# Optimization experiments

Measured on AMD Instinct MI355X. Metric: run time of the kernel, lower is better.

The kernel has to match this reference:

```python
import jax, jax.numpy as jnp
import numpy as np

N_HEADS = 16
LEVELS = 3
DS = 2          # downsampling_factor
WINDOW = 128    # sliding window size
B, L, E = 32, 512, 1024


def _mha(q, k, v, Wq, bq, Wk, bk, Wv, bv, Wo, bo):
    """batch_first nn.MultiheadAttention equivalent (no mask)."""
    b, lq, e = q.shape
    lk = k.shape[1]
    d = e // N_HEADS
    scale = 1.0 / np.sqrt(d)
    qh = (q @ Wq + bq).reshape(b, lq, N_HEADS, d)
    kh = (k @ Wk + bk).reshape(b, lk, N_HEADS, d)
    vh = (v @ Wv + bv).reshape(b, lk, N_HEADS, d)
    att = jax.nn.softmax(jnp.einsum('bqhd,bkhd->bhqk', qh, kh) * scale, axis=-1)
    out = jnp.einsum('bhqk,bkhd->bqhd', att, vh).reshape(b, lq, e)
    return out @ Wo + bo


def _downsample(x):
    b, l, e = x.shape
    ln = l // DS
    return x[:, :ln * DS].reshape(b, ln, DS, e).mean(axis=2)


def setup_inputs() -> dict:
    key = jax.random.key(0)
    ks = jax.random.split(key, 8)
    s = E ** -0.5
    return {
        'query': jax.random.normal(ks[0], (B, L, E), jnp.float32),
        'key': jax.random.normal(ks[1], (B, L, E), jnp.float32),
        'value': jax.random.normal(ks[2], (B, L, E), jnp.float32),
        'Wq': jax.random.normal(ks[3], (E, E), jnp.float32) * s,
        'bq': jnp.zeros((E,), jnp.float32),
        'Wk': jax.random.normal(ks[4], (E, E), jnp.float32) * s,
        'bk': jnp.zeros((E,), jnp.float32),
        'Wv': jax.random.normal(ks[5], (E, E), jnp.float32) * s,
        'bv': jnp.zeros((E,), jnp.float32),
        'Wo': jax.random.normal(ks[6], (E, E), jnp.float32) * s,
        'bo': jnp.zeros((E,), jnp.float32),
        'soft_mask': jnp.ones((L,), jnp.float32),
    }


def reference(query, key, value, Wq, bq, Wk, bk, Wv, bv, Wo, bo, soft_mask):
    params = (Wq, bq, Wk, bk, Wv, bv, Wo, bo)
    # hierarchical multi-scale attention: full KV + (levels-1) downsampled KVs
    k, v = key, value
    acc = _mha(query, k, v, *params)
    for _ in range(LEVELS - 1):
        k = _downsample(k)
        v = _downsample(v)
        acc = acc + _mha(query, k, v, *params)
    hier = acc / LEVELS
    # sliding-window local attention (L divisible by WINDOW)
    b, l, e = query.shape
    nw = l // WINDOW
    qw = query.reshape(b * nw, WINDOW, e)
    kw = key.reshape(b * nw, WINDOW, e)
    vw = value.reshape(b * nw, WINDOW, e)
    sw = _mha(qw, kw, vw, *params).reshape(b, l, e)
    # soft mask gating
    sm = jax.nn.sigmoid(soft_mask[:l])
    return (hier + sw) * sm[None, :, None]
```

## Files before the change

### kernel.cpp

```cpp
#include <hip/hip_runtime.h>

#define EDIM 1024
#define MROWS 16384
#define DHEAD 64
#define LSEQ 512
#define NT 16

typedef unsigned short u16;
typedef unsigned int u32;
typedef __bf16 bf16x8 __attribute__((ext_vector_type(8)));
typedef unsigned short u16x8 __attribute__((ext_vector_type(8)));
typedef float f32x4 __attribute__((ext_vector_type(4)));

__device__ __forceinline__ u16 f2bf(float x) {
    return __builtin_bit_cast(u16, (__bf16)x);
}
__device__ __forceinline__ float bf2f(u16 h) {
    return __builtin_bit_cast(float, (u32)h << 16);
}
__device__ __forceinline__ bf16x8 ld8(const u16* p) {
    return __builtin_bit_cast(bf16x8, *(const u16x8*)p);
}
__device__ __forceinline__ bf16x8 ld8s(const u16* base, int row, int koff) {
    return ld8((const u16*)((const char*)base + row * 128 + ((koff * 2) ^ ((row & 7) << 4))));
}
__device__ __forceinline__ bf16x8 ld8v(const u16* base, int c, int koff) {
    return ld8((const u16*)((const char*)base + c * 128 + ((koff * 2) ^ (((c >> 2) & 7) << 4))));
}
__device__ __forceinline__ void glds16(const u16* g, u16* l) {
    __builtin_amdgcn_global_load_lds(
        (const __attribute__((address_space(1))) u32*)g,
        (__attribute__((address_space(3))) u32*)l, 16, 0, 0);
}
#define MFMA(a, b, c) __builtin_amdgcn_mfma_f32_16x16x32_bf16((a), (b), (c), 0, 0, 0)
#define U4C(v, i) ((i) == 0 ? (v).x : (i) == 1 ? (v).y : (i) == 2 ? (v).z : (v).w)
#define VMCNT(n) asm volatile("s_waitcnt vmcnt(" #n ")" ::: "memory")
#define SBAR()   __builtin_amdgcn_s_barrier()

__global__ __launch_bounds__(256) void prep_wt_kernel(
    const float* __restrict__ Wq, const float* __restrict__ Wk,
    const float* __restrict__ Wv, const float* __restrict__ Wo,
    u16* __restrict__ WTh)
{
    const int z = blockIdx.z;
    const float* W = (z == 0) ? Wq : (z == 1) ? Wk : (z == 2) ? Wv : Wo;
    u16* th = WTh + (size_t)z * EDIM * EDIM;
    const int k0 = blockIdx.x * 64, n0 = blockIdx.y * 64;
    __shared__ float tile[64][65];
    for (int i = threadIdx.x; i < 4096; i += 256) {
        int r = i >> 6, c = i & 63;
        tile[r][c] = W[(size_t)(k0 + r) * EDIM + n0 + c];
    }
    __syncthreads();
    for (int i = threadIdx.x; i < 4096; i += 256) {
        int r = i >> 6, c = i & 63;
        th[(size_t)(n0 + r) * EDIM + k0 + c] = f2bf(tile[c][r]);
    }
}

__global__ __launch_bounds__(256) void convert_kernel(
    const float* __restrict__ Aq, const float* __restrict__ Ak, const float* __restrict__ Av,
    u16* __restrict__ Dq, u16* __restrict__ Dk, u16* __restrict__ Dv)
{
    const int z = blockIdx.z;
    const float* src = (z == 0) ? Aq : (z == 1) ? Ak : Av;
    u16* dst = (z == 0) ? Dq : (z == 1) ? Dk : Dv;
    const size_t total8 = (size_t)MROWS * EDIM / 8;
    for (size_t i = (size_t)blockIdx.x * 256 + threadIdx.x; i < total8;
         i += (size_t)gridDim.x * 256) {
        const float4 a = *(const float4*)&src[i * 8];
        const float4 b = *(const float4*)&src[i * 8 + 4];
        ushort4 h0, h1;
        h0.x = f2bf(a.x); h0.y = f2bf(a.y); h0.z = f2bf(a.z); h0.w = f2bf(a.w);
        h1.x = f2bf(b.x); h1.y = f2bf(b.y); h1.z = f2bf(b.z); h1.w = f2bf(b.w);
        *(ushort4*)&dst[i * 8]     = h0;
        *(ushort4*)&dst[i * 8 + 4] = h1;
    }
}

template<int EPI>
__global__ __launch_bounds__(512, 1) void gemm256(
    const u16* __restrict__ A, const u16* __restrict__ BT,
    const float* __restrict__ bias,
    u16* __restrict__ Ch, float* __restrict__ Cf, const float* __restrict__ smask)
{
    extern __shared__ u16 lds[];
    const int tid = threadIdx.x;
    const int lane = tid & 63, w = tid >> 6;
    const int wm = w >> 2, wn = w & 3;
    const int lr = lane & 15, lg = lane >> 4;
    int D = blockIdx.x;
    int T = (D & 7) * 32 + (D >> 3);
    const int m0 = (T >> 2) * 256, n0 = (T & 3) * 256;

    u16* As0 = lds;
    u16* As1 = lds + 16384;
    u16* Bs0 = lds + 32768;
    u16* Bs1 = lds + 49152;

    auto stageB = [&](int bf, int t) {
        u16* dst = bf ? Bs1 : Bs0;
        #pragma unroll
        for (int c = 0; c < 4; ++c) {
            int idx = tid + c * 512;
            int row = idx >> 3, ch = idx & 7, sch = ch ^ (row & 7);
            glds16(&BT[(size_t)(n0 + row) * EDIM + t * 64 + sch * 8], dst + idx * 8);
        }
    };
    auto stageA = [&](int bf, int t) {
        u16* dst = bf ? As1 : As0;
        #pragma unroll
        for (int c = 0; c < 4; ++c) {
            int idx = tid + c * 512;
            int row = idx >> 3, ch = idx & 7, sch = ch ^ (row & 7);
            glds16(&A[(size_t)(m0 + row) * EDIM + t * 64 + sch * 8], dst + idx * 8);
        }
    };

    f32x4 acc[8][4] = {};
    bf16x8 bf0[4], bf1[4];

    stageB(0, 0);
    stageA(0, 0);
    VMCNT(0);
    SBAR();
    #pragma unroll
    for (int n = 0; n < 4; ++n)
        bf0[n] = ld8s(Bs0, wn * 64 + n * 16 + lr, lg * 8);

    for (int t = 0; t < NT; ++t) {
        const int cur = t & 1;
        u16* Asc = cur ? As1 : As0;
        u16* Bsc = cur ? Bs1 : Bs0;
        u16* Bsn = cur ? Bs0 : Bs1;
        const bool more = (t + 1 < NT);
        bf16x8 af[4];
        #pragma unroll
        for (int mm = 0; mm < 4; ++mm)
            af[mm] = ld8s(Asc, wm * 128 + mm * 16 + lr, lg * 8);
        if (more) { stageB(cur ^ 1, t + 1); stageA(cur ^ 1, t + 1); }
        SBAR();
        __builtin_amdgcn_s_setprio(1);
        #pragma unroll
        for (int n = 0; n < 4; ++n)
            #pragma unroll
            for (int mm = 0; mm < 4; ++mm)
                acc[mm][n] = MFMA(af[mm], bf0[n], acc[mm][n]);
        __builtin_amdgcn_s_setprio(0);
        SBAR();
        bf16x8 ag[4];
        #pragma unroll
        for (int mm = 0; mm < 4; ++mm)
            ag[mm] = ld8s(Asc, wm * 128 + 64 + mm * 16 + lr, lg * 8);
        SBAR();
        __builtin_amdgcn_s_setprio(1);
        #pragma unroll
        for (int n = 0; n < 4; ++n)
            #pragma unroll
            for (int mm = 0; mm < 4; ++mm)
                acc[4 + mm][n] = MFMA(ag[mm], bf0[n], acc[4 + mm][n]);
        __builtin_amdgcn_s_setprio(0);
        SBAR();
        #pragma unroll
        for (int mm = 0; mm < 4; ++mm)
            af[mm] = ld8s(Asc, wm * 128 + mm * 16 + lr, 32 + lg * 8);
        #pragma unroll
        for (int n = 0; n < 4; ++n)
            bf1[n] = ld8s(Bsc, wn * 64 + n * 16 + lr, 32 + lg * 8);
        SBAR();
        __builtin_amdgcn_s_setprio(1);
        #pragma unroll
        for (int n = 0; n < 4; ++n)
            #pragma unroll
            for (int mm = 0; mm < 4; ++mm)
                acc[mm][n] = MFMA(af[mm], bf1[n], acc[mm][n]);
        __builtin_amdgcn_s_setprio(0);
        VMCNT(4);
        SBAR();
        #pragma unroll
        for (int mm = 0; mm < 4; ++mm)
            ag[mm] = ld8s(Asc, wm * 128 + 64 + mm * 16 + lr, 32 + lg * 8);
        if (more) {
            #pragma unroll
            for (int n = 0; n < 4; ++n)
                bf0[n] = ld8s(Bsn, wn * 64 + n * 16 + lr, lg * 8);
        }
        SBAR();
        __builtin_amdgcn_s_setprio(1);
        #pragma unroll
        for (int n = 0; n < 4; ++n)
            #pragma unroll
            for (int mm = 0; mm < 4; ++mm)
                acc[4 + mm][n] = MFMA(ag[mm], bf1[n], acc[4 + mm][n]);
        __builtin_amdgcn_s_setprio(0);
        VMCNT(0);
        SBAR();
    }
    #pragma unroll
    for (int m = 0; m < 8; ++m)
        #pragma unroll
        for (int n = 0; n < 4; ++n) {
            int col = n0 + wn * 64 + n * 16 + lr;
            float bc = bias[col];
            #pragma unroll
            for (int r = 0; r < 4; ++r) {
                int row = m0 + wm * 128 + m * 16 + lg * 4 + r;
                float x = acc[m][n][r];
                if (EPI == 1) {
                    float g = 1.0f / (1.0f + __expf(-smask[row & (LSEQ - 1)]));
                    Cf[(size_t)row * EDIM + col] = (x + 2.0f * bc) * g;
                } else {
                    Ch[(size_t)row * EDIM + col] = f2bf(x + bc);
                }
            }
        }
}

__global__ __launch_bounds__(256, 2) void attn_kernel(
    const u16* __restrict__ Q, const u16* __restrict__ K,
    const u16* __restrict__ V, u16* __restrict__ ctx)
{
    const int tid = threadIdx.x, lane = tid & 63, w = tid >> 6;
    const int lr = lane & 15, lg = lane >> 4;
    int D = (blockIdx.z * gridDim.y + blockIdx.y) * gridDim.x + blockIdx.x;
    int T = (D & 7) * 512 + (D >> 3);
    const int qq = T & 7, hd = (T >> 3) & 15, b = T >> 7;
    const int wrow = b * LSEQ + qq * 64 + w * 16;
    const int ecol = hd * DHEAD;
    const int kvbase = b * LSEQ;
    const int wt0 = qq & ~1;

    __shared__ u16 Ks[2][64 * 64];
    __shared__ u16 Vt[64 * 64];
    __shared__ u16 Ps[4][3 * 16 * 72];

    u16* psw = &Ps[w][0];

    bf16x8 qf0 = ld8(&Q[(size_t)(wrow + lr) * EDIM + ecol + lg * 8]);
    bf16x8 qf1 = ld8(&Q[(size_t)(wrow + lr) * EDIM + ecol + 32 + lg * 8]);

    f32x4 o0[4] = {}, o1[4] = {}, o2[4] = {}, ow[4] = {};
    float l0 = 0, l1 = 0, l2 = 0, lw = 0;
    ushort4 vr[2][2];

    auto issueK = [&](int t, int bf) {
        #pragma unroll
        for (int c = 0; c < 2; ++c) {
            int idx = tid + c * 256;
            int row = idx >> 3, ch = idx & 7;
            int sch = ch ^ (row & 7);
            glds16(&K[(size_t)(kvbase + t * 64 + row) * EDIM + ecol + sch * 8],
                   &Ks[bf][(w * 64 + c * 256) * 8]);
        }
    };
    auto loadV = [&](int t) {
        #pragma unroll
        for (int j = 0; j < 2; ++j) {
            int i4 = tid + j * 256;
            int pr = i4 >> 4, c4 = (i4 & 15) << 2;
            vr[j][0] = *(const ushort4*)&V[(size_t)(kvbase + t * 64 + 2 * pr) * EDIM + ecol + c4];
            vr[j][1] = *(const ushort4*)&V[(size_t)(kvbase + t * 64 + 2 * pr + 1) * EDIM + ecol + c4];
        }
    };
    auto writeV = [&]() {
        #pragma unroll
        for (int j = 0; j < 2; ++j) {
            int i4 = tid + j * 256;
            int pr = i4 >> 4, c4 = (i4 & 15) << 2;
            #pragma unroll
            for (int i = 0; i < 4; ++i) {
                int c = c4 + i;
                int byo = c * 128 + ((4 * pr) ^ (((c >> 2) & 7) << 4));
                *(u32*)((char*)Vt + byo) =
                    (u32)U4C(vr[j][0], i) | ((u32)U4C(vr[j][1], i) << 16);
            }
        }
    };

    int buf = 0;
    issueK(0, 0);
    loadV(0);
    for (int t = 0; t < 8; ++t) {
        __syncthreads();
        writeV();
        __syncthreads();
        if (t < 7) { issueK(t + 1, buf ^ 1); loadV(t + 1); }
        const bool win = (t == wt0) | (t == wt0 + 1);

        float l0t = 0;
        #pragma unroll
        for (int nb = 0; nb < 4; ++nb) {
            bf16x8 kf0 = ld8s(&Ks[buf][0], nb * 16 + lr, lg * 8);
            bf16x8 kf1 = ld8s(&Ks[buf][0], nb * 16 + lr, 32 + lg * 8);
            f32x4 s = {};
            s = MFMA(kf0, qf0, s);
            s = MFMA(kf1, qf1, s);
            s *= 0.125f;
            float p00 = __expf(s[0]), p01 = __expf(s[1]);
            float p02 = __expf(s[2]), p03 = __expf(s[3]);
            float s1a = 0.5f * (s[0] + s[1]), s1b = 0.5f * (s[2] + s[3]);
            float p1a = 0.5f * __expf(s1a), p1b = 0.5f * __expf(s1b);
            float p2v = 0.25f * __expf(0.5f * (s1a + s1b));
            l0t += (p00 + p01) + (p02 + p03);
            l1 += 2.0f * (p1a + p1b);
            l2 += 4.0f * p2v;
            int rb = lr * 144 + nb * 32 + lg * 8;
            *(u32*)((char*)psw + rb)     = (u32)f2bf(p00) | ((u32)f2bf(p01) << 16);
            *(u32*)((char*)psw + rb + 4) = (u32)f2bf(p02) | ((u32)f2bf(p03) << 16);
            u32 w1a = (u32)f2bf(p1a); w1a |= w1a << 16;
            u32 w1b = (u32)f2bf(p1b); w1b |= w1b << 16;
            *(u32*)((char*)psw + 2304 + rb)     = w1a;
            *(u32*)((char*)psw + 2304 + rb + 4) = w1b;
            u32 w2 = (u32)f2bf(p2v); w2 |= w2 << 16;
            *(u32*)((char*)psw + 4608 + rb)     = w2;
            *(u32*)((char*)psw + 4608 + rb + 4) = w2;
        }
        l0 += l0t;
        if (win) lw += l0t;

        bf16x8 pa00 = ld8((const u16*)((char*)psw + lr * 144 + lg * 16));
        bf16x8 pa01 = ld8((const u16*)((char*)psw + lr * 144 + 64 + lg * 16));
        bf16x8 pa10 = ld8((const u16*)((char*)psw + 2304 + lr * 144 + lg * 16));
        bf16x8 pa11 = ld8((const u16*)((char*)psw + 2304 + lr * 144 + 64 + lg * 16));
        bf16x8 pa20 = ld8((const u16*)((char*)psw + 4608 + lr * 144 + lg * 16));
        bf16x8 pa21 = ld8((const u16*)((char*)psw + 4608 + lr * 144 + 64 + lg * 16));
        #pragma unroll
        for (int nd = 0; nd < 4; ++nd) {
            bf16x8 vb0 = ld8v(Vt, nd * 16 + lr, lg * 8);
            bf16x8 vb1 = ld8v(Vt, nd * 16 + lr, 32 + lg * 8);
            o0[nd] = MFMA(pa00, vb0, o0[nd]); o0[nd] = MFMA(pa01, vb1, o0[nd]);
            o1[nd] = MFMA(pa10, vb0, o1[nd]); o1[nd] = MFMA(pa11, vb1, o1[nd]);
            o2[nd] = MFMA(pa20, vb0, o2[nd]); o2[nd] = MFMA(pa21, vb1, o2[nd]);
            if (win) {
                ow[nd] = MFMA(pa00, vb0, ow[nd]);
                ow[nd] = MFMA(pa01, vb1, ow[nd]);
            }
        }
        buf ^= 1;
    }
    l0 += __shfl_xor(l0, 16, 64); l0 += __shfl_xor(l0, 32, 64);
    l1 += __shfl_xor(l1, 16, 64); l1 += __shfl_xor(l1, 32, 64);
    l2 += __shfl_xor(l2, 16, 64); l2 += __shfl_xor(l2, 32, 64);
    lw += __shfl_xor(lw, 16, 64); lw += __shfl_xor(lw, 32, 64);
    float c0 = (1.0f / 3.0f) / l0, c1 = (1.0f / 3.0f) / l1;
    float c2 = (1.0f / 3.0f) / l2, cw = 1.0f / lw;
    #pragma unroll
    for (int r = 0; r < 4; ++r) {
        int src = lg * 4 + r;
        float d0 = __shfl(c0, src, 64);
        float d1 = __shfl(c1, src, 64);
        float d2 = __shfl(c2, src, 64);
        float dw = __shfl(cw, src, 64);
        #pragma unroll
        for (int nd = 0; nd < 4; ++nd) {
            float v = o0[nd][r] * d0 + o1[nd][r] * d1 + o2[nd][r] * d2 + ow[nd][r] * dw;
            ctx[(size_t)(wrow + lg * 4 + r) * EDIM + ecol + nd * 16 + lr] = f2bf(v);
        }
    }
}

extern "C" void kernel_launch(void* const* d_in, const int* in_sizes, int n_in,
                              void* d_out, int out_size, void* d_ws, size_t ws_size,
                              hipStream_t stream)
{
    const float* query = (const float*)d_in[0];
    const float* key   = (const float*)d_in[1];
    const float* value = (const float*)d_in[2];
    const float* Wq = (const float*)d_in[3];
    const float* bq = (const float*)d_in[4];
    const float* Wk = (const float*)d_in[5];
    const float* bk = (const float*)d_in[6];
    const float* Wv = (const float*)d_in[7];
    const float* bv = (const float*)d_in[8];
    const float* Wo = (const float*)d_in[9];
    const float* bo = (const float*)d_in[10];
    const float* smask = (const float*)d_in[11];

    const size_t szWT = (size_t)4 * EDIM * EDIM * 2;
    const size_t szP  = (size_t)MROWS * EDIM * 2;
    const size_t need = szWT + 7 * szP;
    if (ws_size < need) {
        hipMemsetAsync(d_out, 0x7F, (size_t)out_size * 4, stream);
        return;
    }
    size_t off = 0;
    auto take = [&](size_t n) -> void* {
        void* p = (char*)d_ws + off;
        off += (n + 255) & ~(size_t)255;
        return p;
    };
    u16* WTh = (u16*)take(szWT);
    u16* Aq  = (u16*)take(szP);
    u16* Ak  = (u16*)take(szP);
    u16* Av  = (u16*)take(szP);
    u16* Qh  = (u16*)take(szP);
    u16* Kh  = (u16*)take(szP);
    u16* Vh  = (u16*)take(szP);
    u16* ctx = (u16*)take(szP);

    hipFuncSetAttribute(reinterpret_cast<const void*>(gemm256<0>),
                        hipFuncAttributeMaxDynamicSharedMemorySize, 131072);
    hipFuncSetAttribute(reinterpret_cast<const void*>(gemm256<1>),
                        hipFuncAttributeMaxDynamicSharedMemorySize, 131072);

    prep_wt_kernel<<<dim3(16, 16, 4), 256, 0, stream>>>(Wq, Wk, Wv, Wo, WTh);
    convert_kernel<<<dim3(4096, 1, 3), 256, 0, stream>>>(query, key, value, Aq, Ak, Av);

    gemm256<0><<<256, 512, 131072, stream>>>(
        Aq, WTh + 0 * (size_t)EDIM * EDIM, bq, Qh, nullptr, nullptr);
    gemm256<0><<<256, 512, 131072, stream>>>(
        Ak, WTh + 1 * (size_t)EDIM * EDIM, bk, Kh, nullptr, nullptr);
    gemm256<0><<<256, 512, 131072, stream>>>(
        Av, WTh + 2 * (size_t)EDIM * EDIM, bv, Vh, nullptr, nullptr);

    attn_kernel<<<dim3(8, 16, 32), 256, 0, stream>>>(Qh, Kh, Vh, ctx);

    gemm256<1><<<256, 512, 131072, stream>>>(
        ctx, WTh + 3 * (size_t)EDIM * EDIM, bo, nullptr, (float*)d_out, smask);
}
```

Measured before the change: 377.7 us.

## Process two Q row tiles per attention wave and fold softmax scale into Wq

The attention kernel now gives each wave 32 query rows (two 16-row tiles) instead of 16, so each block covers 128 query rows. Every K tile staged in LDS and every V fragment read from LDS is reused across both tiles, and the grid is halved to 2048 blocks with dynamic shared memory. The scale 0.125*log2(e) is folded into Wq and bq so the kernel can call exp2f directly and drop the per-score multiply. The pooled-level weights move into the final normalisation constants. The cost is more registers and more LDS per block, which may lower occupancy.

```diff
diff --git a/kernel.cpp b/kernel.cpp
--- a/kernel.cpp
+++ b/kernel.cpp
@@ -5,6 +5,7 @@
 #define DHEAD 64
 #define LSEQ 512
 #define NT 16
+#define QSCL 0.18033688011112042f
 
 typedef unsigned short u16;
 typedef unsigned int u32;
@@ -31,6 +32,12 @@
     __builtin_amdgcn_global_load_lds(
         (const __attribute__((address_space(1))) u32*)g,
         (__attribute__((address_space(3))) u32*)l, 16, 0, 0);
+}
+__device__ __forceinline__ u32 pk2(float a, float b) {
+    return (u32)f2bf(a) | ((u32)f2bf(b) << 16);
+}
+__device__ __forceinline__ u32 dup2(float a) {
+    u32 v = (u32)f2bf(a); return v | (v << 16);
 }
 #define MFMA(a, b, c) __builtin_amdgcn_mfma_f32_16x16x32_bf16((a), (b), (c), 0, 0, 0)
 #define U4C(v, i) ((i) == 0 ? (v).x : (i) == 1 ? (v).y : (i) == 2 ? (v).z : (v).w)
@@ -44,6 +51,7 @@
 {
     const int z = blockIdx.z;
     const float* W = (z == 0) ? Wq : (z == 1) ? Wk : (z == 2) ? Wv : Wo;
+    const float scl = (z == 0) ? QSCL : 1.0f;
     u16* th = WTh + (size_t)z * EDIM * EDIM;
     const int k0 = blockIdx.x * 64, n0 = blockIdx.y * 64;
     __shared__ float tile[64][65];
@@ -54,7 +62,7 @@
     __syncthreads();
     for (int i = threadIdx.x; i < 4096; i += 256) {
         int r = i >> 6, c = i & 63;
-        th[(size_t)(n0 + r) * EDIM + k0 + c] = f2bf(tile[c][r]);
+        th[(size_t)(n0 + r) * EDIM + k0 + c] = f2bf(tile[c][r] * scl);
     }
 }
 
@@ -81,7 +89,7 @@
 template<int EPI>
 __global__ __launch_bounds__(512, 1) void gemm256(
     const u16* __restrict__ A, const u16* __restrict__ BT,
-    const float* __restrict__ bias,
+    const float* __restrict__ bias, float bsc,
     u16* __restrict__ Ch, float* __restrict__ Cf, const float* __restrict__ smask)
 {
     extern __shared__ u16 lds[];
@@ -210,7 +218,7 @@
                     float g = 1.0f / (1.0f + __expf(-smask[row & (LSEQ - 1)]));
                     Cf[(size_t)row * EDIM + col] = (x + 2.0f * bc) * g;
                 } else {
-                    Ch[(size_t)row * EDIM + col] = f2bf(x + bc);
+                    Ch[(size_t)row * EDIM + col] = f2bf(x + bsc * bc);
                 }
             }
         }
@@ -220,37 +228,42 @@
     const u16* __restrict__ Q, const u16* __restrict__ K,
     const u16* __restrict__ V, u16* __restrict__ ctx)
 {
+    extern __shared__ u16 alds[];
     const int tid = threadIdx.x, lane = tid & 63, w = tid >> 6;
     const int lr = lane & 15, lg = lane >> 4;
-    int D = (blockIdx.z * gridDim.y + blockIdx.y) * gridDim.x + blockIdx.x;
-    int T = (D & 7) * 512 + (D >> 3);
-    const int qq = T & 7, hd = (T >> 3) & 15, b = T >> 7;
-    const int wrow = b * LSEQ + qq * 64 + w * 16;
+    int D = blockIdx.x;
+    int T = (D & 7) * 256 + (D >> 3);
+    const int qq = T & 3, hd = (T >> 2) & 15, b = T >> 6;
+    const int wrow = b * LSEQ + qq * 128 + w * 32;
     const int ecol = hd * DHEAD;
     const int kvbase = b * LSEQ;
-    const int wt0 = qq & ~1;
-
-    __shared__ u16 Ks[2][64 * 64];
-    __shared__ u16 Vt[64 * 64];
-    __shared__ u16 Ps[4][3 * 16 * 72];
-
-    u16* psw = &Ps[w][0];
-
-    bf16x8 qf0 = ld8(&Q[(size_t)(wrow + lr) * EDIM + ecol + lg * 8]);
-    bf16x8 qf1 = ld8(&Q[(size_t)(wrow + lr) * EDIM + ecol + 32 + lg * 8]);
-
-    f32x4 o0[4] = {}, o1[4] = {}, o2[4] = {}, ow[4] = {};
-    float l0 = 0, l1 = 0, l2 = 0, lw = 0;
+    const int wt0 = qq * 2;
+
+    u16* Ks0 = alds;
+    u16* Ks1 = alds + 4096;
+    u16* Vt  = alds + 8192;
+    char* psw = (char*)(alds + 12288) + w * 13824;
+
+    bf16x8 qf[2][2];
+    #pragma unroll
+    for (int m = 0; m < 2; ++m)
+        #pragma unroll
+        for (int ks = 0; ks < 2; ++ks)
+            qf[m][ks] = ld8(&Q[(size_t)(wrow + m * 16 + lr) * EDIM + ecol + ks * 32 + lg * 8]);
+
+    f32x4 o0[2][4] = {}, o1[2][4] = {}, o2[2][4] = {}, ow[2][4] = {};
+    float l0[2] = {}, l1[2] = {}, l2[2] = {}, lw[2] = {};
     ushort4 vr[2][2];
 
     auto issueK = [&](int t, int bf) {
+        u16* dst = bf ? Ks1 : Ks0;
         #pragma unroll
         for (int c = 0; c < 2; ++c) {
             int idx = tid + c * 256;
             int row = idx >> 3, ch = idx & 7;
             int sch = ch ^ (row & 7);
             glds16(&K[(size_t)(kvbase + t * 64 + row) * EDIM + ecol + sch * 8],
-                   &Ks[bf][(w * 64 + c * 256) * 8]);
+                   dst + idx * 8);
         }
     };
     auto loadV = [&](int t) {
@@ -286,75 +299,93 @@
         __syncthreads();
         if (t < 7) { issueK(t + 1, buf ^ 1); loadV(t + 1); }
         const bool win = (t == wt0) | (t == wt0 + 1);
-
-        float l0t = 0;
+        u16* Ksc = buf ? Ks1 : Ks0;
+
+        float l0t[2] = {};
         #pragma unroll
         for (int nb = 0; nb < 4; ++nb) {
-            bf16x8 kf0 = ld8s(&Ks[buf][0], nb * 16 + lr, lg * 8);
-            bf16x8 kf1 = ld8s(&Ks[buf][0], nb * 16 + lr, 32 + lg * 8);
-            f32x4 s = {};
-            s = MFMA(kf0, qf0, s);
-            s = MFMA(kf1, qf1, s);
-            s *= 0.125f;
-            float p00 = __expf(s[0]), p01 = __expf(s[1]);
-            float p02 = __expf(s[2]), p03 = __expf(s[3]);
-            float s1a = 0.5f * (s[0] + s[1]), s1b = 0.5f * (s[2] + s[3]);
-            float p1a = 0.5f * __expf(s1a), p1b = 0.5f * __expf(s1b);
-            float p2v = 0.25f * __expf(0.5f * (s1a + s1b));
-            l0t += (p00 + p01) + (p02 + p03);
-            l1 += 2.0f * (p1a + p1b);
-            l2 += 4.0f * p2v;
-            int rb = lr * 144 + nb * 32 + lg * 8;
-            *(u32*)((char*)psw + rb)     = (u32)f2bf(p00) | ((u32)f2bf(p01) << 16);
-            *(u32*)((char*)psw + rb + 4) = (u32)f2bf(p02) | ((u32)f2bf(p03) << 16);
-            u32 w1a = (u32)f2bf(p1a); w1a |= w1a << 16;
-            u32 w1b = (u32)f2bf(p1b); w1b |= w1b << 16;
-            *(u32*)((char*)psw + 2304 + rb)     = w1a;
-            *(u32*)((char*)psw + 2304 + rb + 4) = w1b;
-            u32 w2 = (u32)f2bf(p2v); w2 |= w2 << 16;
-            *(u32*)((char*)psw + 4608 + rb)     = w2;
-            *(u32*)((char*)psw + 4608 + rb + 4) = w2;
-        }
-        l0 += l0t;
-        if (win) lw += l0t;
-
-        bf16x8 pa00 = ld8((const u16*)((char*)psw + lr * 144 + lg * 16));
-        bf16x8 pa01 = ld8((const u16*)((char*)psw + lr * 144 + 64 + lg * 16));
-        bf16x8 pa10 = ld8((const u16*)((char*)psw + 2304 + lr * 144 + lg * 16));
-        bf16x8 pa11 = ld8((const u16*)((char*)psw + 2304 + lr * 144 + 64 + lg * 16));
-        bf16x8 pa20 = ld8((const u16*)((char*)psw + 4608 + lr * 144 + lg * 16));
-        bf16x8 pa21 = ld8((const u16*)((char*)psw + 4608 + lr * 144 + 64 + lg * 16));
+            bf16x8 kf0 = ld8s(Ksc, nb * 16 + lr, lg * 8);
+            bf16x8 kf1 = ld8s(Ksc, nb * 16 + lr, 32 + lg * 8);
+            #pragma unroll
+            for (int m = 0; m < 2; ++m) {
+                f32x4 s = {};
+                s = MFMA(kf0, qf[m][0], s);
+                s = MFMA(kf1, qf[m][1], s);
+                float p00 = exp2f(s[0]), p01 = exp2f(s[1]);
+                float p02 = exp2f(s[2]), p03 = exp2f(s[3]);
+                float s1a = 0.5f * (s[0] + s[1]), s1b = 0.5f * (s[2] + s[3]);
+                float p1a = exp2f(s1a), p1b = exp2f(s1b);
+                float p2v = exp2f(0.5f * (s1a + s1b));
+                l0t[m] += (p00 + p01) + (p02 + p03);
+                l1[m] += p1a + p1b;
+                l2[m] += p2v;
+                char* pb = psw + (m * 16 + lr) * 144 + nb * 32 + lg * 8;
+                *(u32*)pb           = pk2(p00, p01);
+                *(u32*)(pb + 4)     = pk2(p02, p03);
+                *(u32*)(pb + 4608)  = dup2(p1a);
+                *(u32*)(pb + 4612)  = dup2(p1b);
+                u32 w2 = dup2(p2v);
+                *(u32*)(pb + 9216)  = w2;
+                *(u32*)(pb + 9220)  = w2;
+            }
+        }
+        l0[0] += l0t[0]; l0[1] += l0t[1];
+        if (win) { lw[0] += l0t[0]; lw[1] += l0t[1]; }
+
+        bf16x8 vb[4][2];
         #pragma unroll
         for (int nd = 0; nd < 4; ++nd) {
-            bf16x8 vb0 = ld8v(Vt, nd * 16 + lr, lg * 8);
-            bf16x8 vb1 = ld8v(Vt, nd * 16 + lr, 32 + lg * 8);
-            o0[nd] = MFMA(pa00, vb0, o0[nd]); o0[nd] = MFMA(pa01, vb1, o0[nd]);
-            o1[nd] = MFMA(pa10, vb0, o1[nd]); o1[nd] = MFMA(pa11, vb1, o1[nd]);
-            o2[nd] = MFMA(pa20, vb0, o2[nd]); o2[nd] = MFMA(pa21, vb1, o2[nd]);
-            if (win) {
-                ow[nd] = MFMA(pa00, vb0, ow[nd]);
-                ow[nd] = MFMA(pa01, vb1, ow[nd]);
+            vb[nd][0] = ld8v(Vt, nd * 16 + lr, lg * 8);
+            vb[nd][1] = ld8v(Vt, nd * 16 + lr, 32 + lg * 8);
+        }
+        #pragma unroll
+        for (int m = 0; m < 2; ++m) {
+            char* pb = psw + (m * 16 + lr) * 144;
+            bf16x8 pa00 = ld8((const u16*)(pb + lg * 16));
+            bf16x8 pa01 = ld8((const u16*)(pb + 64 + lg * 16));
+            bf16x8 pa10 = ld8((const u16*)(pb + 4608 + lg * 16));
+            bf16x8 pa11 = ld8((const u16*)(pb + 4672 + lg * 16));
+            bf16x8 pa20 = ld8((const u16*)(pb + 9216 + lg * 16));
+            bf16x8 pa21 = ld8((const u16*)(pb + 9280 + lg * 16));
+            #pragma unroll
+            for (int nd = 0; nd < 4; ++nd) {
+                o0[m][nd] = MFMA(pa00, vb[nd][0], o0[m][nd]);
+                o0[m][nd] = MFMA(pa01, vb[nd][1], o0[m][nd]);
+                o1[m][nd] = MFMA(pa10, vb[nd][0], o1[m][nd]);
+                o1[m][nd] = MFMA(pa11, vb[nd][1], o1[m][nd]);
+                o2[m][nd] = MFMA(pa20, vb[nd][0], o2[m][nd]);
+                o2[m][nd] = MFMA(pa21, vb[nd][1], o2[m][nd]);
+                if (win) {
+                    ow[m][nd] = MFMA(pa00, vb[nd][0], ow[m][nd]);
+                    ow[m][nd] = MFMA(pa01, vb[nd][1], ow[m][nd]);
+                }
             }
         }
         buf ^= 1;
     }
-    l0 += __shfl_xor(l0, 16, 64); l0 += __shfl_xor(l0, 32, 64);
-    l1 += __shfl_xor(l1, 16, 64); l1 += __shfl_xor(l1, 32, 64);
-    l2 += __shfl_xor(l2, 16, 64); l2 += __shfl_xor(l2, 32, 64);
-    lw += __shfl_xor(lw, 16, 64); lw += __shfl_xor(lw, 32, 64);
-    float c0 = (1.0f / 3.0f) / l0, c1 = (1.0f / 3.0f) / l1;
-    float c2 = (1.0f / 3.0f) / l2, cw = 1.0f / lw;
     #pragma unroll
-    for (int r = 0; r < 4; ++r) {
-        int src = lg * 4 + r;
-        float d0 = __shfl(c0, src, 64);
-        float d1 = __shfl(c1, src, 64);
-        float d2 = __shfl(c2, src, 64);
-        float dw = __shfl(cw, src, 64);
-        #pragma unroll
-        for (int nd = 0; nd < 4; ++nd) {
-            float v = o0[nd][r] * d0 + o1[nd][r] * d1 + o2[nd][r] * d2 + ow[nd][r] * dw;
-            ctx[(size_t)(wrow + lg * 4 + r) * EDIM + ecol + nd * 16 + lr] = f2bf(v);
+    for (int m = 0; m < 2; ++m) {
+        l0[m] += __shfl_xor(l0[m], 16, 64); l0[m] += __shfl_xor(l0[m], 32, 64);
+        l1[m] += __shfl_xor(l1[m], 16, 64); l1[m] += __shfl_xor(l1[m], 32, 64);
+        l2[m] += __shfl_xor(l2[m], 16, 64); l2[m] += __shfl_xor(l2[m], 32, 64);
+        lw[m] += __shfl_xor(lw[m], 16, 64); lw[m] += __shfl_xor(lw[m], 32, 64);
+        float c0 = (1.0f / 3.0f) / l0[m];
+        float c1 = (1.0f / 6.0f) / l1[m];
+        float c2 = (1.0f / 12.0f) / l2[m];
+        float cw = 1.0f / lw[m];
+        #pragma unroll
+        for (int r = 0; r < 4; ++r) {
+            int src = lg * 4 + r;
+            float d0 = __shfl(c0, src, 64);
+            float d1 = __shfl(c1, src, 64);
+            float d2 = __shfl(c2, src, 64);
+            float dw = __shfl(cw, src, 64);
+            #pragma unroll
+            for (int nd = 0; nd < 4; ++nd) {
+                float v = o0[m][nd][r] * d0 + o1[m][nd][r] * d1
+                        + o2[m][nd][r] * d2 + ow[m][nd][r] * dw;
+                ctx[(size_t)(wrow + m * 16 + lg * 4 + r) * EDIM + ecol + nd * 16 + lr] = f2bf(v);
+            }
         }
     }
 }
@@ -398,23 +429,25 @@
     u16* Vh  = (u16*)take(szP);
     u16* ctx = (u16*)take(szP);
 
-    hipFuncSetAttribute(reinterpret_cast<const void*>(gemm256<0>),
-                        hipFuncAttributeMaxDynamicSharedMemorySize, 131072);
-    hipFuncSetAttribute(reinterpret_cast<const void*>(gemm256<1>),
-                        hipFuncAttributeMaxDynamicSharedMemorySize, 131072);
+    (void)hipFuncSetAttribute(reinterpret_cast<const void*>(gemm256<0>),
+                              hipFuncAttributeMaxDynamicSharedMemorySize, 131072);
+    (void)hipFuncSetAttribute(reinterpret_cast<const void*>(gemm256<1>),
+                              hipFuncAttributeMaxDynamicSharedMemorySize, 131072);
+    (void)hipFuncSetAttribute(reinterpret_cast<const void*>(attn_kernel),
+                              hipFuncAttributeMaxDynamicSharedMemorySize, 81920);
 
     prep_wt_kernel<<<dim3(16, 16, 4), 256, 0, stream>>>(Wq, Wk, Wv, Wo, WTh);
     convert_kernel<<<dim3(4096, 1, 3), 256, 0, stream>>>(query, key, value, Aq, Ak, Av);
 
     gemm256<0><<<256, 512, 131072, stream>>>(
-        Aq, WTh + 0 * (size_t)EDIM * EDIM, bq, Qh, nullptr, nullptr);
+        Aq, WTh + 0 * (size_t)EDIM * EDIM, bq, QSCL, Qh, nullptr, nullptr);
     gemm256<0><<<256, 512, 131072, stream>>>(
-        Ak, WTh + 1 * (size_t)EDIM * EDIM, bk, Kh, nullptr, nullptr);
+        Ak, WTh + 1 * (size_t)EDIM * EDIM, bk, 1.0f, Kh, nullptr, nullptr);
     gemm256<0><<<256, 512, 131072, stream>>>(
-        Av, WTh + 2 * (size_t)EDIM * EDIM, bv, Vh, nullptr, nullptr);
-
-    attn_kernel<<<dim3(8, 16, 32), 256, 0, stream>>>(Qh, Kh, Vh, ctx);
+        Av, WTh + 2 * (size_t)EDIM * EDIM, bv, 1.0f, Vh, nullptr, nullptr);
+
+    attn_kernel<<<2048, 256, 79872, stream>>>(Qh, Kh, Vh, ctx);
 
     gemm256<1><<<256, 512, 131072, stream>>>(
-        ctx, WTh + 3 * (size_t)EDIM * EDIM, bo, nullptr, (float*)d_out, smask);
-}
+        ctx, WTh + 3 * (size_t)EDIM * EDIM, bo, 1.0f, nullptr, (float*)d_out, smask);
+}
```

Result: slower. 454.3 us (+20.3%).

## Fold softmax scale into Wq and restructure attention into 512-thread blocks with sequential P buffers

Applied to the files above, without the earlier changes.

The 1/sqrt(d) scale is folded into the bf16 Wq weights and the Q bias, which removes a per-score multiply in attention. The attention kernel moves to 512-thread blocks covering 128 query rows, so each K/V tile staged in LDS is shared by twice as many waves. The three per-level probability tiles are now written and consumed one after another through a single per-wave buffer instead of three, which cuts LDS per block and should allow more resident blocks. The factors of 0.5 and 0.25 on the pooled-level probabilities move into the final normalization constants. In exchange there are extra intra-wave LDS write/read round-trips, and rounding Q*0.125 to bf16 changes numerics slightly.

```diff
diff --git a/kernel.cpp b/kernel.cpp
--- a/kernel.cpp
+++ b/kernel.cpp
@@ -5,6 +5,7 @@
 #define DHEAD 64
 #define LSEQ 512
 #define NT 16
+#define QSCL 0.125f
 
 typedef unsigned short u16;
 typedef unsigned int u32;
@@ -31,6 +32,12 @@
     __builtin_amdgcn_global_load_lds(
         (const __attribute__((address_space(1))) u32*)g,
         (__attribute__((address_space(3))) u32*)l, 16, 0, 0);
+}
+__device__ __forceinline__ u32 pk2(float a, float b) {
+    return (u32)f2bf(a) | ((u32)f2bf(b) << 16);
+}
+__device__ __forceinline__ u32 dup2(float a) {
+    u32 v = (u32)f2bf(a); return v | (v << 16);
 }
 #define MFMA(a, b, c) __builtin_amdgcn_mfma_f32_16x16x32_bf16((a), (b), (c), 0, 0, 0)
 #define U4C(v, i) ((i) == 0 ? (v).x : (i) == 1 ? (v).y : (i) == 2 ? (v).z : (v).w)
@@ -44,6 +51,7 @@
 {
     const int z = blockIdx.z;
     const float* W = (z == 0) ? Wq : (z == 1) ? Wk : (z == 2) ? Wv : Wo;
+    const float scl = (z == 0) ? QSCL : 1.0f;
     u16* th = WTh + (size_t)z * EDIM * EDIM;
     const int k0 = blockIdx.x * 64, n0 = blockIdx.y * 64;
     __shared__ float tile[64][65];
@@ -54,7 +62,7 @@
     __syncthreads();
     for (int i = threadIdx.x; i < 4096; i += 256) {
         int r = i >> 6, c = i & 63;
-        th[(size_t)(n0 + r) * EDIM + k0 + c] = f2bf(tile[c][r]);
+        th[(size_t)(n0 + r) * EDIM + k0 + c] = f2bf(tile[c][r] * scl);
     }
 }
 
@@ -81,7 +89,7 @@
 template<int EPI>
 __global__ __launch_bounds__(512, 1) void gemm256(
     const u16* __restrict__ A, const u16* __restrict__ BT,
-    const float* __restrict__ bias,
+    const float* __restrict__ bias, float bsc,
     u16* __restrict__ Ch, float* __restrict__ Cf, const float* __restrict__ smask)
 {
     extern __shared__ u16 lds[];
@@ -210,70 +218,55 @@
                     float g = 1.0f / (1.0f + __expf(-smask[row & (LSEQ - 1)]));
                     Cf[(size_t)row * EDIM + col] = (x + 2.0f * bc) * g;
                 } else {
-                    Ch[(size_t)row * EDIM + col] = f2bf(x + bc);
+                    Ch[(size_t)row * EDIM + col] = f2bf(x + bsc * bc);
                 }
             }
         }
 }
 
-__global__ __launch_bounds__(256, 2) void attn_kernel(
+__global__ __launch_bounds__(512, 4) void attn_kernel(
     const u16* __restrict__ Q, const u16* __restrict__ K,
     const u16* __restrict__ V, u16* __restrict__ ctx)
 {
+    __shared__ u16 Ks[2][64 * 64];
+    __shared__ u16 Vt[64 * 64];
+    __shared__ u16 Ps[8][16 * 72];
     const int tid = threadIdx.x, lane = tid & 63, w = tid >> 6;
     const int lr = lane & 15, lg = lane >> 4;
-    int D = (blockIdx.z * gridDim.y + blockIdx.y) * gridDim.x + blockIdx.x;
-    int T = (D & 7) * 512 + (D >> 3);
-    const int qq = T & 7, hd = (T >> 3) & 15, b = T >> 7;
-    const int wrow = b * LSEQ + qq * 64 + w * 16;
+    int D = blockIdx.x;
+    int T = (D & 7) * 256 + (D >> 3);
+    const int qq = T & 3, hd = (T >> 2) & 15, b = T >> 6;
+    const int wrow = b * LSEQ + qq * 128 + w * 16;
     const int ecol = hd * DHEAD;
     const int kvbase = b * LSEQ;
-    const int wt0 = qq & ~1;
-
-    __shared__ u16 Ks[2][64 * 64];
-    __shared__ u16 Vt[64 * 64];
-    __shared__ u16 Ps[4][3 * 16 * 72];
-
-    u16* psw = &Ps[w][0];
+    const int wt0 = qq * 2;
+
+    char* psw = (char*)&Ps[w][0];
 
     bf16x8 qf0 = ld8(&Q[(size_t)(wrow + lr) * EDIM + ecol + lg * 8]);
     bf16x8 qf1 = ld8(&Q[(size_t)(wrow + lr) * EDIM + ecol + 32 + lg * 8]);
 
     f32x4 o0[4] = {}, o1[4] = {}, o2[4] = {}, ow[4] = {};
     float l0 = 0, l1 = 0, l2 = 0, lw = 0;
-    ushort4 vr[2][2];
+    ushort4 vr0, vr1;
 
     auto issueK = [&](int t, int bf) {
-        #pragma unroll
-        for (int c = 0; c < 2; ++c) {
-            int idx = tid + c * 256;
-            int row = idx >> 3, ch = idx & 7;
-            int sch = ch ^ (row & 7);
-            glds16(&K[(size_t)(kvbase + t * 64 + row) * EDIM + ecol + sch * 8],
-                   &Ks[bf][(w * 64 + c * 256) * 8]);
-        }
+        int row = tid >> 3, ch = tid & 7, sch = ch ^ (row & 7);
+        glds16(&K[(size_t)(kvbase + t * 64 + row) * EDIM + ecol + sch * 8],
+               &Ks[bf][w * 512]);
     };
     auto loadV = [&](int t) {
-        #pragma unroll
-        for (int j = 0; j < 2; ++j) {
-            int i4 = tid + j * 256;
-            int pr = i4 >> 4, c4 = (i4 & 15) << 2;
-            vr[j][0] = *(const ushort4*)&V[(size_t)(kvbase + t * 64 + 2 * pr) * EDIM + ecol + c4];
-            vr[j][1] = *(const ushort4*)&V[(size_t)(kvbase + t * 64 + 2 * pr + 1) * EDIM + ecol + c4];
-        }
+        int pr = tid >> 4, c4 = (tid & 15) << 2;
+        vr0 = *(const ushort4*)&V[(size_t)(kvbase + t * 64 + 2 * pr) * EDIM + ecol + c4];
+        vr1 = *(const ushort4*)&V[(size_t)(kvbase + t * 64 + 2 * pr + 1) * EDIM + ecol + c4];
     };
     auto writeV = [&]() {
-        #pragma unroll
-        for (int j = 0; j < 2; ++j) {
-            int i4 = tid + j * 256;
-            int pr = i4 >> 4, c4 = (i4 & 15) << 2;
-            #pragma unroll
-            for (int i = 0; i < 4; ++i) {
-                int c = c4 + i;
-                int byo = c * 128 + ((4 * pr) ^ (((c >> 2) & 7) << 4));
-                *(u32*)((char*)Vt + byo) =
-                    (u32)U4C(vr[j][0], i) | ((u32)U4C(vr[j][1], i) << 16);
-            }
+        int pr = tid >> 4, c4 = (tid & 15) << 2;
+        #pragma unroll
+        for (int i = 0; i < 4; ++i) {
+            int c = c4 + i;
+            int byo = c * 128 + ((4 * pr) ^ (((c >> 2) & 7) << 4));
+            *(u32*)((char*)Vt + byo) = (u32)U4C(vr0, i) | ((u32)U4C(vr1, i) << 16);
         }
     };
 
@@ -286,54 +279,85 @@
         __syncthreads();
         if (t < 7) { issueK(t + 1, buf ^ 1); loadV(t + 1); }
         const bool win = (t == wt0) | (t == wt0 + 1);
-
+        u16* Ksc = &Ks[buf][0];
+
+        f32x4 s[4];
+        #pragma unroll
+        for (int nb = 0; nb < 4; ++nb) {
+            bf16x8 kf0 = ld8s(Ksc, nb * 16 + lr, lg * 8);
+            bf16x8 kf1 = ld8s(Ksc, nb * 16 + lr, 32 + lg * 8);
+            f32x4 a = {};
+            a = MFMA(kf0, qf0, a);
+            a = MFMA(kf1, qf1, a);
+            s[nb] = a;
+        }
         float l0t = 0;
         #pragma unroll
         for (int nb = 0; nb < 4; ++nb) {
-            bf16x8 kf0 = ld8s(&Ks[buf][0], nb * 16 + lr, lg * 8);
-            bf16x8 kf1 = ld8s(&Ks[buf][0], nb * 16 + lr, 32 + lg * 8);
-            f32x4 s = {};
-            s = MFMA(kf0, qf0, s);
-            s = MFMA(kf1, qf1, s);
-            s *= 0.125f;
-            float p00 = __expf(s[0]), p01 = __expf(s[1]);
-            float p02 = __expf(s[2]), p03 = __expf(s[3]);
-            float s1a = 0.5f * (s[0] + s[1]), s1b = 0.5f * (s[2] + s[3]);
-            float p1a = 0.5f * __expf(s1a), p1b = 0.5f * __expf(s1b);
-            float p2v = 0.25f * __expf(0.5f * (s1a + s1b));
-            l0t += (p00 + p01) + (p02 + p03);
-            l1 += 2.0f * (p1a + p1b);
-            l2 += 4.0f * p2v;
-            int rb = lr * 144 + nb * 32 + lg * 8;
-            *(u32*)((char*)psw + rb)     = (u32)f2bf(p00) | ((u32)f2bf(p01) << 16);
-            *(u32*)((char*)psw + rb + 4) = (u32)f2bf(p02) | ((u32)f2bf(p03) << 16);
-            u32 w1a = (u32)f2bf(p1a); w1a |= w1a << 16;
-            u32 w1b = (u32)f2bf(p1b); w1b |= w1b << 16;
-            *(u32*)((char*)psw + 2304 + rb)     = w1a;
-            *(u32*)((char*)psw + 2304 + rb + 4) = w1b;
-            u32 w2 = (u32)f2bf(p2v); w2 |= w2 << 16;
-            *(u32*)((char*)psw + 4608 + rb)     = w2;
-            *(u32*)((char*)psw + 4608 + rb + 4) = w2;
+            float p0 = __expf(s[nb][0]), p1 = __expf(s[nb][1]);
+            float p2 = __expf(s[nb][2]), p3 = __expf(s[nb][3]);
+            l0t += (p0 + p1) + (p2 + p3);
+            char* pb = psw + lr * 144 + nb * 32 + lg * 8;
+            *(u32*)pb       = pk2(p0, p1);
+            *(u32*)(pb + 4) = pk2(p2, p3);
         }
         l0 += l0t;
         if (win) lw += l0t;
-
-        bf16x8 pa00 = ld8((const u16*)((char*)psw + lr * 144 + lg * 16));
-        bf16x8 pa01 = ld8((const u16*)((char*)psw + lr * 144 + 64 + lg * 16));
-        bf16x8 pa10 = ld8((const u16*)((char*)psw + 2304 + lr * 144 + lg * 16));
-        bf16x8 pa11 = ld8((const u16*)((char*)psw + 2304 + lr * 144 + 64 + lg * 16));
-        bf16x8 pa20 = ld8((const u16*)((char*)psw + 4608 + lr * 144 + lg * 16));
-        bf16x8 pa21 = ld8((const u16*)((char*)psw + 4608 + lr * 144 + 64 + lg * 16));
-        #pragma unroll
-        for (int nd = 0; nd < 4; ++nd) {
-            bf16x8 vb0 = ld8v(Vt, nd * 16 + lr, lg * 8);
-            bf16x8 vb1 = ld8v(Vt, nd * 16 + lr, 32 + lg * 8);
-            o0[nd] = MFMA(pa00, vb0, o0[nd]); o0[nd] = MFMA(pa01, vb1, o0[nd]);
-            o1[nd] = MFMA(pa10, vb0, o1[nd]); o1[nd] = MFMA(pa11, vb1, o1[nd]);
-            o2[nd] = MFMA(pa20, vb0, o2[nd]); o2[nd] = MFMA(pa21, vb1, o2[nd]);
-            if (win) {
-                ow[nd] = MFMA(pa00, vb0, ow[nd]);
-                ow[nd] = MFMA(pa01, vb1, ow[nd]);
+        {
+            bf16x8 pa0 = ld8((const u16*)(psw + lr * 144 + lg * 16));
+            bf16x8 pa1 = ld8((const u16*)(psw + lr * 144 + 64 + lg * 16));
+            #pragma unroll
+            for (int nd = 0; nd < 4; ++nd) {
+                bf16x8 vb0 = ld8v(Vt, nd * 16 + lr, lg * 8);
+                bf16x8 vb1 = ld8v(Vt, nd * 16 + lr, 32 + lg * 8);
+                o0[nd] = MFMA(pa0, vb0, o0[nd]);
+                o0[nd] = MFMA(pa1, vb1, o0[nd]);
+                if (win) {
+                    ow[nd] = MFMA(pa0, vb0, ow[nd]);
+                    ow[nd] = MFMA(pa1, vb1, ow[nd]);
+                }
+            }
+        }
+        float s1[4][2];
+        #pragma unroll
+        for (int nb = 0; nb < 4; ++nb) {
+            s1[nb][0] = 0.5f * (s[nb][0] + s[nb][1]);
+            s1[nb][1] = 0.5f * (s[nb][2] + s[nb][3]);
+            float pa = __expf(s1[nb][0]), pc = __expf(s1[nb][1]);
+            l1 += pa + pc;
+            char* pb = psw + lr * 144 + nb * 32 + lg * 8;
+            *(u32*)pb       = dup2(pa);
+            *(u32*)(pb + 4) = dup2(pc);
+        }
+        {
+            bf16x8 pa0 = ld8((const u16*)(psw + lr * 144 + lg * 16));
+            bf16x8 pa1 = ld8((const u16*)(psw + lr * 144 + 64 + lg * 16));
+            #pragma unroll
+            for (int nd = 0; nd < 4; ++nd) {
+                bf16x8 vb0 = ld8v(Vt, nd * 16 + lr, lg * 8);
+                bf16x8 vb1 = ld8v(Vt, nd * 16 + lr, 32 + lg * 8);
+                o1[nd] = MFMA(pa0, vb0, o1[nd]);
+                o1[nd] = MFMA(pa1, vb1, o1[nd]);
+            }
+        }
+        #pragma unroll
+        for (int nb = 0; nb < 4; ++nb) {
+            float pv = __expf(0.5f * (s1[nb][0] + s1[nb][1]));
+            l2 += pv;
+            char* pb = psw + lr * 144 + nb * 32 + lg * 8;
+            u32 d = dup2(pv);
+            *(u32*)pb       = d;
+            *(u32*)(pb + 4) = d;
+        }
+        {
+            bf16x8 pa0 = ld8((const u16*)(psw + lr * 144 + lg * 16));
+            bf16x8 pa1 = ld8((const u16*)(psw + lr * 144 + 64 + lg * 16));
+            #pragma unroll
+            for (int nd = 0; nd < 4; ++nd) {
+                bf16x8 vb0 = ld8v(Vt, nd * 16 + lr, lg * 8);
+                bf16x8 vb1 = ld8v(Vt, nd * 16 + lr, 32 + lg * 8);
+                o2[nd] = MFMA(pa0, vb0, o2[nd]);
+                o2[nd] = MFMA(pa1, vb1, o2[nd]);
             }
         }
         buf ^= 1;
@@ -342,8 +366,10 @@
     l1 += __shfl_xor(l1, 16, 64); l1 += __shfl_xor(l1, 32, 64);
     l2 += __shfl_xor(l2, 16, 64); l2 += __shfl_xor(l2, 32, 64);
     lw += __shfl_xor(lw, 16, 64); lw += __shfl_xor(lw, 32, 64);
-    float c0 = (1.0f / 3.0f) / l0, c1 = (1.0f / 3.0f) / l1;
-    float c2 = (1.0f / 3.0f) / l2, cw = 1.0f / lw;
+    float c0 = (1.0f / 3.0f) / l0;
+    float c1 = (1.0f / 6.0f) / l1;
+    float c2 = (1.0f / 12.0f) / l2;
+    float cw = 1.0f / lw;
     #pragma unroll
     for (int r = 0; r < 4; ++r) {
         int src = lg * 4 + r;
@@ -398,23 +424,23 @@
     u16* Vh  = (u16*)take(szP);
     u16* ctx = (u16*)take(szP);
 
-    hipFuncSetAttribute(reinterpret_cast<const void*>(gemm256<0>),
-                        hipFuncAttributeMaxDynamicSharedMemorySize, 131072);
-    hipFuncSetAttribute(reinterpret_cast<const void*>(gemm256<1>),
-                        hipFuncAttributeMaxDynamicSharedMemorySize, 131072);
+    (void)hipFuncSetAttribute(reinterpret_cast<const void*>(gemm256<0>),
+                              hipFuncAttributeMaxDynamicSharedMemorySize, 131072);
+    (void)hipFuncSetAttribute(reinterpret_cast<const void*>(gemm256<1>),
+                              hipFuncAttributeMaxDynamicSharedMemorySize, 131072);
 
     prep_wt_kernel<<<dim3(16, 16, 4), 256, 0, stream>>>(Wq, Wk, Wv, Wo, WTh);
     convert_kernel<<<dim3(4096, 1, 3), 256, 0, stream>>>(query, key, value, Aq, Ak, Av);
 
     gemm256<0><<<256, 512, 131072, stream>>>(
-        Aq, WTh + 0 * (size_t)EDIM * EDIM, bq, Qh, nullptr, nullptr);
+        Aq, WTh + 0 * (size_t)EDIM * EDIM, bq, QSCL, Qh, nullptr, nullptr);
     gemm256<0><<<256, 512, 131072, stream>>>(
-        Ak, WTh + 1 * (size_t)EDIM * EDIM, bk, Kh, nullptr, nullptr);
+        Ak, WTh + 1 * (size_t)EDIM * EDIM, bk, 1.0f, Kh, nullptr, nullptr);
     gemm256<0><<<256, 512, 131072, stream>>>(
-        Av, WTh + 2 * (size_t)EDIM * EDIM, bv, Vh, nullptr, nullptr);
-
-    attn_kernel<<<dim3(8, 16, 32), 256, 0, stream>>>(Qh, Kh, Vh, ctx);
+        Av, WTh + 2 * (size_t)EDIM * EDIM, bv, 1.0f, Vh, nullptr, nullptr);
+
+    attn_kernel<<<2048, 512, 0, stream>>>(Qh, Kh, Vh, ctx);
 
     gemm256<1><<<256, 512, 131072, stream>>>(
-        ctx, WTh + 3 * (size_t)EDIM * EDIM, bo, nullptr, (float*)d_out, smask);
-}
+        ctx, WTh + 3 * (size_t)EDIM * EDIM, bo, 1.0f, nullptr, (float*)d_out, smask);
+}
```

Result: slower. 536.8 us (+42.1%).
